# Performance work log

Hardware: AMD Instinct MI355X
Metric: run time of the kernel (lower is better)

Reference implementation:

```python
import jax, jax.numpy as jnp
import numpy as np
from jax import lax

SAMPLE_RATE = 44100.0

def _shelf_coeffs(gain_db, fc, q, sr, high):
    # RBJ cookbook shelf biquad; high=True -> high_shelf, else low_shelf
    A = 10.0 ** (gain_db / 40.0)
    w0 = 2.0 * jnp.pi * (fc / sr)
    alpha = jnp.sin(w0) / (2.0 * q)
    c = jnp.cos(w0)
    sA = jnp.sqrt(A)
    sgn = 1.0 if high else -1.0
    b0 = A * (A + 1 + sgn * (A - 1) * c + 2 * sA * alpha)
    b1 = -2.0 * sgn * A * (A - 1 + sgn * (A + 1) * c)
    b2 = A * (A + 1 + sgn * (A - 1) * c - 2 * sA * alpha)
    a0 = A + 1 - sgn * (A - 1) * c + 2 * sA * alpha
    a1 = 2.0 * sgn * (A - 1 - sgn * (A + 1) * c)
    a2 = A + 1 - sgn * (A - 1) * c - 2 * sA * alpha
    b = jnp.stack([b0, b1, b2]) / a0
    a = jnp.stack([a0, a1, a2]) / a0
    return b, a

def _peaking_coeffs(gain_db, fc, q, sr):
    A = 10.0 ** (gain_db / 40.0)
    w0 = 2.0 * jnp.pi * (fc / sr)
    alpha = jnp.sin(w0) / (2.0 * q)
    c = jnp.cos(w0)
    b0 = 1 + alpha * A
    b1 = -2.0 * c
    b2 = 1 - alpha * A
    a0 = 1 + alpha / A
    a1 = -2.0 * c
    a2 = 1 - alpha / A
    b = jnp.stack([b0, b1, b2]) / a0
    a = jnp.stack([a0, a1, a2]) / a0
    return b, a

def _biquad_lfilter(b, a, x):
    # scipy.signal.lfilter with zero initial conditions, transposed DF-II.
    # x: (chs, T); state s: (chs, 2)
    b0, b1, b2 = b[0], b[1], b[2]
    a1, a2 = a[1], a[2]
    def step(s, xn):  # xn: (chs,)
        s1, s2 = s[:, 0], s[:, 1]
        yn = b0 * xn + s1
        s1n = b1 * xn - a1 * yn + s2
        s2n = b2 * xn - a2 * yn
        return jnp.stack([s1n, s2n], axis=1), yn
    s0 = jnp.zeros((x.shape[0], 2), x.dtype)
    _, y = lax.scan(step, s0, x.T)  # y: (T, chs)
    return y.T

def setup_inputs() -> dict:
    key = jax.random.key(0)
    x = jax.random.normal(key, (8, 2097152), dtype=jnp.float32)
    # rows: [low_shelf, band1, band2, band3, high_shelf]; cols: [gain_db, cutoff_hz, Q]
    eq_params = jnp.array([
        [3.0, 100.0, 0.9],
        [-2.5, 400.0, 1.2],
        [4.0, 1000.0, 2.0],
        [-5.0, 4000.0, 0.7],
        [2.5, 12000.0, 0.707],
    ], dtype=jnp.float32)
    return {"x": x, "eq_params": eq_params}

def reference(x, eq_params):
    sr = SAMPLE_RATE
    # low shelf
    b, a = _shelf_coeffs(eq_params[0, 0], eq_params[0, 1], eq_params[0, 2], sr, high=False)
    y = _biquad_lfilter(b, a, x)
    # 3 peaking bands
    for i in range(1, 4):
        b, a = _peaking_coeffs(eq_params[i, 0], eq_params[i, 1], eq_params[i, 2], sr)
        y = _biquad_lfilter(b, a, y)
    # high shelf
    b, a = _shelf_coeffs(eq_params[4, 0], eq_params[4, 1], eq_params[4, 2], sr, high=True)
    y = _biquad_lfilter(b, a, y)
    return y.astype(jnp.float32)
```

## Files before the change

kernel.cpp:

```cpp
#include <hip/hip_runtime.h>

#define SRATE 44100.0
#ifndef M_PI
#define M_PI 3.14159265358979323846
#endif

#define THREADS 256
#define NBLK 2048
#define STRIDE 17

__device__ __forceinline__ void matvec_tri(const float* __restrict__ M,
                                           const float* bs, float* acc) {
    #pragma unroll
    for (int i = 0; i < 5; i++) {
        #pragma unroll
        for (int h = 0; h < 2; h++) {
            const int r = 2*i + h;
            float a = acc[r];
            #pragma unroll
            for (int k = 0; k < 2*i + 2; k++)
                a = fmaf(M[r*10 + k], bs[k], a);
            acc[r] = a;
        }
    }
}

__device__ __forceinline__ float cascade5(const float* cb0, const float* cb1,
                                          const float* cb2, const float* ca1,
                                          const float* ca2, float* s, float u) {
    #pragma unroll
    for (int st = 0; st < 5; st++) {
        float y  = fmaf(cb0[st], u, s[2*st]);
        float t1 = fmaf(cb1[st], u, s[2*st+1]);
        s[2*st+1] = fmaf(-ca2[st], y, cb2[st] * u);
        s[2*st]   = fmaf(-ca1[st], y, t1);
        u = y;
    }
    return u;
}

__global__ __launch_bounds__(128) void k0_setup(const float* __restrict__ eqp,
                                                float* __restrict__ coef_f,
                                                float* __restrict__ mats_f) {
    __shared__ double cfd[25];
    __shared__ double Md[100];
    int t = threadIdx.x;

    if (t < 5) {
        int i = t;
        double g  = (double)eqp[i*3 + 0];
        double fc = (double)eqp[i*3 + 1];
        double q  = (double)eqp[i*3 + 2];
        double A  = pow(10.0, g / 40.0);
        double w0 = 2.0 * M_PI * (fc / SRATE);
        double al = sin(w0) / (2.0 * q);
        double c  = cos(w0);
        double b0, b1, b2, a0, a1, a2;
        if (i == 0 || i == 4) {
            double sgn = (i == 4) ? 1.0 : -1.0;
            double sA = sqrt(A);
            b0 = A * ((A + 1.0) + sgn * (A - 1.0) * c + 2.0 * sA * al);
            b1 = -2.0 * sgn * A * ((A - 1.0) + sgn * (A + 1.0) * c);
            b2 = A * ((A + 1.0) + sgn * (A - 1.0) * c - 2.0 * sA * al);
            a0 = (A + 1.0) - sgn * (A - 1.0) * c + 2.0 * sA * al;
            a1 = 2.0 * sgn * ((A - 1.0) - sgn * (A + 1.0) * c);
            a2 = (A + 1.0) - sgn * (A - 1.0) * c - 2.0 * sA * al;
        } else {
            b0 = 1.0 + al * A; b1 = -2.0 * c; b2 = 1.0 - al * A;
            a0 = 1.0 + al / A; a1 = -2.0 * c; a2 = 1.0 - al / A;
        }
        cfd[i*5+0] = b0/a0; cfd[i*5+1] = b1/a0; cfd[i*5+2] = b2/a0;
        cfd[i*5+3] = a1/a0; cfd[i*5+4] = a2/a0;
        coef_f[i*5+0] = (float)(b0/a0); coef_f[i*5+1] = (float)(b1/a0);
        coef_f[i*5+2] = (float)(b2/a0); coef_f[i*5+3] = (float)(a1/a0);
        coef_f[i*5+4] = (float)(a2/a0);
    }
    __syncthreads();

    if (t < 10) {
        double s[10];
        #pragma unroll
        for (int k = 0; k < 10; k++) s[k] = (k == t) ? 1.0 : 0.0;
        double u = 0.0;
        #pragma unroll
        for (int i = 0; i < 5; i++) {
            double y   = cfd[i*5+0] * u + s[2*i];
            double s1n = cfd[i*5+1] * u - cfd[i*5+3] * y + s[2*i+1];
            double s2n = cfd[i*5+2] * u - cfd[i*5+4] * y;
            s[2*i] = s1n; s[2*i+1] = s2n; u = y;
        }
        for (int r = 0; r < 10; r++) Md[r*10 + t] = s[r];
    }
    __syncthreads();

    for (int k = 1; k <= 20; k++) {
        double val = 0.0;
        if (t < 100) {
            int r = t / 10, c = t % 10;
            #pragma unroll
            for (int j = 0; j < 10; j++) val += Md[r*10 + j] * Md[j*10 + c];
        }
        __syncthreads();
        if (t < 100) {
            Md[t] = val;
            int d = k - 5;
            if (d >= 0 && d < 16) mats_f[d*100 + t] = (float)val;
        }
        __syncthreads();
    }
}

__global__ __launch_bounds__(256, 6) void kA(const float* __restrict__ x,
                                             const float* __restrict__ coef,
                                             const float* __restrict__ mats,
                                             float* __restrict__ ibuf,
                                             float* __restrict__ abuf) {
    __shared__ union {
        float stage[256 * STRIDE];
        float buf[256][11];
    } sm;
    __shared__ float Mf[800];
    __shared__ float cfs[25];
    const int t = threadIdx.x, b = blockIdx.x;
    const int cb = t >> 2, q = t & 3;
    const float4* x4 = (const float4*)x + (size_t)b * 2048;

    float4 rr[4];
    #pragma unroll
    for (int k = 0; k < 4; k++) rr[k] = x4[(cb + 64*k)*8 + q];

    for (int i = t; i < 800; i += 256) Mf[i] = mats[i];
    if (t < 25) cfs[t] = coef[t];

    #pragma unroll
    for (int k = 0; k < 4; k++) {
        int o = (cb + 64*k)*STRIDE + q*4;
        sm.stage[o+0]=rr[k].x; sm.stage[o+1]=rr[k].y;
        sm.stage[o+2]=rr[k].z; sm.stage[o+3]=rr[k].w;
    }
    __syncthreads();

    #pragma unroll
    for (int k = 0; k < 4; k++) rr[k] = x4[(cb + 64*k)*8 + 4 + q];

    float cb0[5],cb1[5],cb2[5],ca1[5],ca2[5];
    #pragma unroll
    for (int i = 0; i < 5; i++) {
        cb0[i]=cfs[i*5+0]; cb1[i]=cfs[i*5+1]; cb2[i]=cfs[i*5+2];
        ca1[i]=cfs[i*5+3]; ca2[i]=cfs[i*5+4];
    }

    float s[10];
    #pragma unroll
    for (int k = 0; k < 10; k++) s[k] = 0.0f;

    {
        const float* row = sm.stage + t*STRIDE;
        #pragma unroll
        for (int i = 0; i < 16; i++) (void)cascade5(cb0,cb1,cb2,ca1,ca2, s, row[i]);
    }
    __syncthreads();
    #pragma unroll
    for (int k = 0; k < 4; k++) {
        int o = (cb + 64*k)*STRIDE + q*4;
        sm.stage[o+0]=rr[k].x; sm.stage[o+1]=rr[k].y;
        sm.stage[o+2]=rr[k].z; sm.stage[o+3]=rr[k].w;
    }
    __syncthreads();
    {
        const float* row = sm.stage + t*STRIDE;
        #pragma unroll
        for (int i = 0; i < 16; i++) (void)cascade5(cb0,cb1,cb2,ca1,ca2, s, row[i]);
    }
    __syncthreads();

    #pragma unroll
    for (int r = 0; r < 10; r++) sm.buf[t][r] = s[r];
    __syncthreads();

    #pragma unroll 1
    for (int d = 0; d < 8; d++) {
        int src = t - (1 << d);
        int sc  = src < 0 ? 0 : src;
        float bs[10], nv[10];
        #pragma unroll
        for (int r = 0; r < 10; r++) { bs[r] = sm.buf[sc][r]; nv[r] = s[r]; }
        matvec_tri(&Mf[d*100], bs, nv);
        __syncthreads();
        bool act = src >= 0;
        #pragma unroll
        for (int r = 0; r < 10; r++) { s[r] = act ? nv[r] : s[r]; sm.buf[t][r] = s[r]; }
        __syncthreads();
    }

    #pragma unroll
    for (int r = 0; r < 10; r++)
        ibuf[(size_t)b * 2560 + r * 256 + t] = (t > 0) ? sm.buf[t-1][r] : 0.0f;
    if (t == 255) {
        #pragma unroll
        for (int r = 0; r < 10; r++) abuf[b * 10 + r] = s[r];
    }
}

__global__ __launch_bounds__(256) void kB(const float* __restrict__ mats,
                                          const float* __restrict__ abuf,
                                          float* __restrict__ bbuf) {
    __shared__ float Qf[800];
    __shared__ float buf[256][11];
    const int t = threadIdx.x, ch = blockIdx.x;
    const int g = ch * 256 + t;

    for (int i = t; i < 800; i += 256) Qf[i] = mats[800 + i];

    float v[10];
    #pragma unroll
    for (int r = 0; r < 10; r++) { v[r] = abuf[g * 10 + r]; buf[t][r] = v[r]; }
    __syncthreads();

    #pragma unroll 1
    for (int e = 0; e < 8; e++) {
        int src = t - (1 << e);
        int sc  = src < 0 ? 0 : src;
        float bs[10], nv[10];
        #pragma unroll
        for (int r = 0; r < 10; r++) { bs[r] = buf[sc][r]; nv[r] = v[r]; }
        matvec_tri(&Qf[e*100], bs, nv);
        __syncthreads();
        bool act = src >= 0;
        #pragma unroll
        for (int r = 0; r < 10; r++) { v[r] = act ? nv[r] : v[r]; buf[t][r] = v[r]; }
        __syncthreads();
    }

    #pragma unroll
    for (int r = 0; r < 10; r++)
        bbuf[g * 10 + r] = (t > 0) ? buf[t-1][r] : 0.0f;
}

__global__ __launch_bounds__(256, 6) void kC(const float* __restrict__ x,
                                             const float* __restrict__ coef,
                                             const float* __restrict__ mats,
                                             const float* __restrict__ ibuf,
                                             const float* __restrict__ bbuf,
                                             float* __restrict__ out) {
    __shared__ float stage[256 * STRIDE];
    __shared__ float Mf[800];
    __shared__ float cfs[25];
    const int t = threadIdx.x, b = blockIdx.x;
    const int cb = t >> 2, q = t & 3;
    const float4* x4 = (const float4*)x + (size_t)b * 2048;
    float4* o4 = (float4*)out + (size_t)b * 2048;

    float4 rr[4];
    #pragma unroll
    for (int k = 0; k < 4; k++) rr[k] = x4[(cb + 64*k)*8 + q];

    float sp[10];
    #pragma unroll
    for (int r = 0; r < 10; r++) sp[r] = ibuf[(size_t)b * 2560 + r * 256 + t];
    float bp[10];
    #pragma unroll
    for (int r = 0; r < 10; r++) bp[r] = bbuf[b * 10 + r];

    for (int i = t; i < 800; i += 256) Mf[i] = mats[i];
    if (t < 25) cfs[t] = coef[t];

    #pragma unroll
    for (int k = 0; k < 4; k++) {
        int o = (cb + 64*k)*STRIDE + q*4;
        stage[o+0]=rr[k].x; stage[o+1]=rr[k].y;
        stage[o+2]=rr[k].z; stage[o+3]=rr[k].w;
    }
    __syncthreads();

    #pragma unroll
    for (int k = 0; k < 4; k++) rr[k] = x4[(cb + 64*k)*8 + 4 + q];

    float cb0[5],cb1[5],cb2[5],ca1[5],ca2[5];
    #pragma unroll
    for (int i = 0; i < 5; i++) {
        cb0[i]=cfs[i*5+0]; cb1[i]=cfs[i*5+1]; cb2[i]=cfs[i*5+2];
        ca1[i]=cfs[i*5+3]; ca2[i]=cfs[i*5+4];
    }

    #pragma unroll 1
    for (int d = 0; d < 8; d++) {
        float wv[10];
        #pragma unroll
        for (int r = 0; r < 10; r++) wv[r] = 0.0f;
        matvec_tri(&Mf[d*100], bp, wv);
        bool bit = (t >> d) & 1;
        #pragma unroll
        for (int r = 0; r < 10; r++) bp[r] = bit ? wv[r] : bp[r];
    }
    float s[10];
    #pragma unroll
    for (int r = 0; r < 10; r++) s[r] = sp[r] + bp[r];

    {
        float* row = stage + t*STRIDE;
        #pragma unroll
        for (int i = 0; i < 16; i++) row[i] = cascade5(cb0,cb1,cb2,ca1,ca2, s, row[i]);
    }
    __syncthreads();
    #pragma unroll
    for (int k = 0; k < 4; k++) {
        int o = (cb + 64*k)*STRIDE + q*4;
        o4[(cb + 64*k)*8 + q] = make_float4(stage[o+0], stage[o+1], stage[o+2], stage[o+3]);
    }
    __syncthreads();
    #pragma unroll
    for (int k = 0; k < 4; k++) {
        int o = (cb + 64*k)*STRIDE + q*4;
        stage[o+0]=rr[k].x; stage[o+1]=rr[k].y;
        stage[o+2]=rr[k].z; stage[o+3]=rr[k].w;
    }
    __syncthreads();
    {
        float* row = stage + t*STRIDE;
        #pragma unroll
        for (int i = 0; i < 16; i++) row[i] = cascade5(cb0,cb1,cb2,ca1,ca2, s, row[i]);
    }
    __syncthreads();
    #pragma unroll
    for (int k = 0; k < 4; k++) {
        int o = (cb + 64*k)*STRIDE + q*4;
        o4[(cb + 64*k)*8 + 4 + q] = make_float4(stage[o+0], stage[o+1], stage[o+2], stage[o+3]);
    }
}

extern "C" void kernel_launch(void* const* d_in, const int* in_sizes, int n_in,
                              void* d_out, int out_size, void* d_ws, size_t ws_size,
                              hipStream_t stream) {
    const float* x   = (const float*)d_in[0];
    const float* eqp = (const float*)d_in[1];
    float* out = (float*)d_out;
    char* ws = (char*)d_ws;

    float* coef_f = (float*)ws;
    float* mats_f = (float*)(ws + 256);
    float* ibuf   = (float*)(ws + 8192);
    float* abuf   = (float*)(ws + 8192 + 20971520);
    float* bbuf   = (float*)(ws + 8192 + 20971520 + 81920);

    hipLaunchKernelGGL(k0_setup, dim3(1), dim3(128), 0, stream, eqp, coef_f, mats_f);
    hipLaunchKernelGGL(kA, dim3(NBLK), dim3(THREADS), 0, stream, x, coef_f, mats_f, ibuf, abuf);
    hipLaunchKernelGGL(kB, dim3(8),    dim3(THREADS), 0, stream, mats_f, abuf, bbuf);
    hipLaunchKernelGGL(kC, dim3(NBLK), dim3(THREADS), 0, stream,
                       x, coef_f, mats_f, ibuf, bbuf, out);
}
```

Baseline: 190.1 us.

## Recompute intra-block prefix states in kC instead of round-tripping ibuf

kA no longer writes the per-thread exclusive prefix states (about 20 MB) to global memory. Its block-level scan becomes a reduction-only up-sweep that produces just the block aggregate. kC now reruns the local cascade and the full Hillis-Steele scan itself, keeping input in registers to avoid a second global read, and writes output through a double shared-memory stage with fewer barriers. This removes a large global write and read in exchange for duplicated compute in kC, more registers, more shared memory, and a lower launch-bounds occupancy hint.

```diff
diff --git a/kernel.cpp b/kernel.cpp
--- a/kernel.cpp
+++ b/kernel.cpp
@@ -110,24 +110,26 @@
     }
 }
 
-__global__ __launch_bounds__(256, 6) void kA(const float* __restrict__ x,
+__global__ __launch_bounds__(256, 4) void kA(const float* __restrict__ x,
                                              const float* __restrict__ coef,
                                              const float* __restrict__ mats,
-                                             float* __restrict__ ibuf,
                                              float* __restrict__ abuf) {
     __shared__ union {
-        float stage[256 * STRIDE];
+        float s0[256 * STRIDE];
         float buf[256][11];
-    } sm;
+    } smA;
+    __shared__ float s1[256 * STRIDE];
     __shared__ float Mf[800];
     __shared__ float cfs[25];
     const int t = threadIdx.x, b = blockIdx.x;
     const int cb = t >> 2, q = t & 3;
     const float4* x4 = (const float4*)x + (size_t)b * 2048;
 
-    float4 rr[4];
-    #pragma unroll
-    for (int k = 0; k < 4; k++) rr[k] = x4[(cb + 64*k)*8 + q];
+    float4 rr[4], rr2[4];
+    #pragma unroll
+    for (int k = 0; k < 4; k++) rr[k]  = x4[(cb + 64*k)*8 + q];
+    #pragma unroll
+    for (int k = 0; k < 4; k++) rr2[k] = x4[(cb + 64*k)*8 + 4 + q];
 
     for (int i = t; i < 800; i += 256) Mf[i] = mats[i];
     if (t < 25) cfs[t] = coef[t];
@@ -135,13 +137,17 @@
     #pragma unroll
     for (int k = 0; k < 4; k++) {
         int o = (cb + 64*k)*STRIDE + q*4;
-        sm.stage[o+0]=rr[k].x; sm.stage[o+1]=rr[k].y;
-        sm.stage[o+2]=rr[k].z; sm.stage[o+3]=rr[k].w;
-    }
-    __syncthreads();
-
-    #pragma unroll
-    for (int k = 0; k < 4; k++) rr[k] = x4[(cb + 64*k)*8 + 4 + q];
+        smA.s0[o+0]=rr[k].x; smA.s0[o+1]=rr[k].y;
+        smA.s0[o+2]=rr[k].z; smA.s0[o+3]=rr[k].w;
+    }
+    __syncthreads();
+
+    #pragma unroll
+    for (int k = 0; k < 4; k++) {
+        int o = (cb + 64*k)*STRIDE + q*4;
+        s1[o+0]=rr2[k].x; s1[o+1]=rr2[k].y;
+        s1[o+2]=rr2[k].z; s1[o+3]=rr2[k].w;
+    }
 
     float cb0[5],cb1[5],cb2[5],ca1[5],ca2[5];
     #pragma unroll
@@ -154,48 +160,35 @@
     #pragma unroll
     for (int k = 0; k < 10; k++) s[k] = 0.0f;
 
-    {
-        const float* row = sm.stage + t*STRIDE;
+    {   const float* row = smA.s0 + t*STRIDE;
         #pragma unroll
         for (int i = 0; i < 16; i++) (void)cascade5(cb0,cb1,cb2,ca1,ca2, s, row[i]);
     }
     __syncthreads();
-    #pragma unroll
-    for (int k = 0; k < 4; k++) {
-        int o = (cb + 64*k)*STRIDE + q*4;
-        sm.stage[o+0]=rr[k].x; sm.stage[o+1]=rr[k].y;
-        sm.stage[o+2]=rr[k].z; sm.stage[o+3]=rr[k].w;
-    }
-    __syncthreads();
-    {
-        const float* row = sm.stage + t*STRIDE;
+    {   const float* row = s1 + t*STRIDE;
         #pragma unroll
         for (int i = 0; i < 16; i++) (void)cascade5(cb0,cb1,cb2,ca1,ca2, s, row[i]);
     }
-    __syncthreads();
-
-    #pragma unroll
-    for (int r = 0; r < 10; r++) sm.buf[t][r] = s[r];
+
+    #pragma unroll
+    for (int r = 0; r < 10; r++) smA.buf[t][r] = s[r];
     __syncthreads();
 
     #pragma unroll 1
     for (int d = 0; d < 8; d++) {
-        int src = t - (1 << d);
-        int sc  = src < 0 ? 0 : src;
-        float bs[10], nv[10];
-        #pragma unroll
-        for (int r = 0; r < 10; r++) { bs[r] = sm.buf[sc][r]; nv[r] = s[r]; }
-        matvec_tri(&Mf[d*100], bs, nv);
-        __syncthreads();
-        bool act = src >= 0;
-        #pragma unroll
-        for (int r = 0; r < 10; r++) { s[r] = act ? nv[r] : s[r]; sm.buf[t][r] = s[r]; }
-        __syncthreads();
-    }
-
-    #pragma unroll
-    for (int r = 0; r < 10; r++)
-        ibuf[(size_t)b * 2560 + r * 256 + t] = (t > 0) ? sm.buf[t-1][r] : 0.0f;
+        const int span = 2 << d;
+        if (((t + 1) & (span - 1)) == 0) {
+            const int partner = t - (1 << d);
+            float bs[10];
+            #pragma unroll
+            for (int r = 0; r < 10; r++) bs[r] = smA.buf[partner][r];
+            matvec_tri(&Mf[d*100], bs, s);
+            #pragma unroll
+            for (int r = 0; r < 10; r++) smA.buf[t][r] = s[r];
+        }
+        __syncthreads();
+    }
+
     if (t == 255) {
         #pragma unroll
         for (int r = 0; r < 10; r++) abuf[b * 10 + r] = s[r];
@@ -237,13 +230,16 @@
         bbuf[g * 10 + r] = (t > 0) ? buf[t-1][r] : 0.0f;
 }
 
-__global__ __launch_bounds__(256, 6) void kC(const float* __restrict__ x,
+__global__ __launch_bounds__(256, 4) void kC(const float* __restrict__ x,
                                              const float* __restrict__ coef,
                                              const float* __restrict__ mats,
-                                             const float* __restrict__ ibuf,
                                              const float* __restrict__ bbuf,
                                              float* __restrict__ out) {
-    __shared__ float stage[256 * STRIDE];
+    __shared__ union {
+        float s0[256 * STRIDE];
+        float buf[256][11];
+    } smA;
+    __shared__ float s1[256 * STRIDE];
     __shared__ float Mf[800];
     __shared__ float cfs[25];
     const int t = threadIdx.x, b = blockIdx.x;
@@ -251,30 +247,33 @@
     const float4* x4 = (const float4*)x + (size_t)b * 2048;
     float4* o4 = (float4*)out + (size_t)b * 2048;
 
-    float4 rr[4];
-    #pragma unroll
-    for (int k = 0; k < 4; k++) rr[k] = x4[(cb + 64*k)*8 + q];
-
-    float sp[10];
-    #pragma unroll
-    for (int r = 0; r < 10; r++) sp[r] = ibuf[(size_t)b * 2560 + r * 256 + t];
-    float bp[10];
-    #pragma unroll
-    for (int r = 0; r < 10; r++) bp[r] = bbuf[b * 10 + r];
+    float4 rr[4], rr2[4];
+    #pragma unroll
+    for (int k = 0; k < 4; k++) rr[k]  = x4[(cb + 64*k)*8 + q];
+    #pragma unroll
+    for (int k = 0; k < 4; k++) rr2[k] = x4[(cb + 64*k)*8 + 4 + q];
 
     for (int i = t; i < 800; i += 256) Mf[i] = mats[i];
     if (t < 25) cfs[t] = coef[t];
 
+    float bp[10];
+    #pragma unroll
+    for (int r = 0; r < 10; r++) bp[r] = bbuf[b * 10 + r];
+
     #pragma unroll
     for (int k = 0; k < 4; k++) {
         int o = (cb + 64*k)*STRIDE + q*4;
-        stage[o+0]=rr[k].x; stage[o+1]=rr[k].y;
-        stage[o+2]=rr[k].z; stage[o+3]=rr[k].w;
-    }
-    __syncthreads();
-
-    #pragma unroll
-    for (int k = 0; k < 4; k++) rr[k] = x4[(cb + 64*k)*8 + 4 + q];
+        smA.s0[o+0]=rr[k].x; smA.s0[o+1]=rr[k].y;
+        smA.s0[o+2]=rr[k].z; smA.s0[o+3]=rr[k].w;
+    }
+    __syncthreads();
+
+    #pragma unroll
+    for (int k = 0; k < 4; k++) {
+        int o = (cb + 64*k)*STRIDE + q*4;
+        s1[o+0]=rr2[k].x; s1[o+1]=rr2[k].y;
+        s1[o+2]=rr2[k].z; s1[o+3]=rr2[k].w;
+    }
 
     float cb0[5],cb1[5],cb2[5],ca1[5],ca2[5];
     #pragma unroll
@@ -283,6 +282,43 @@
         ca1[i]=cfs[i*5+3]; ca2[i]=cfs[i*5+4];
     }
 
+    float xw0[16], xw1[16];
+    float s[10];
+    #pragma unroll
+    for (int k = 0; k < 10; k++) s[k] = 0.0f;
+    {   const float* row = smA.s0 + t*STRIDE;
+        #pragma unroll
+        for (int i = 0; i < 16; i++) { xw0[i] = row[i]; (void)cascade5(cb0,cb1,cb2,ca1,ca2, s, xw0[i]); }
+    }
+    __syncthreads();
+    {   const float* row = s1 + t*STRIDE;
+        #pragma unroll
+        for (int i = 0; i < 16; i++) { xw1[i] = row[i]; (void)cascade5(cb0,cb1,cb2,ca1,ca2, s, xw1[i]); }
+    }
+
+    #pragma unroll
+    for (int r = 0; r < 10; r++) smA.buf[t][r] = s[r];
+    __syncthreads();
+
+    #pragma unroll 1
+    for (int d = 0; d < 8; d++) {
+        int src = t - (1 << d);
+        int sc  = src < 0 ? 0 : src;
+        float bs[10], nv[10];
+        #pragma unroll
+        for (int r = 0; r < 10; r++) { bs[r] = smA.buf[sc][r]; nv[r] = s[r]; }
+        matvec_tri(&Mf[d*100], bs, nv);
+        __syncthreads();
+        bool act = src >= 0;
+        #pragma unroll
+        for (int r = 0; r < 10; r++) { s[r] = act ? nv[r] : s[r]; smA.buf[t][r] = s[r]; }
+        __syncthreads();
+    }
+
+    float sp[10];
+    #pragma unroll
+    for (int r = 0; r < 10; r++) sp[r] = (t > 0) ? smA.buf[t-1][r] : 0.0f;
+
     #pragma unroll 1
     for (int d = 0; d < 8; d++) {
         float wv[10];
@@ -293,39 +329,32 @@
         #pragma unroll
         for (int r = 0; r < 10; r++) bp[r] = bit ? wv[r] : bp[r];
     }
-    float s[10];
     #pragma unroll
     for (int r = 0; r < 10; r++) s[r] = sp[r] + bp[r];
-
-    {
-        float* row = stage + t*STRIDE;
-        #pragma unroll
-        for (int i = 0; i < 16; i++) row[i] = cascade5(cb0,cb1,cb2,ca1,ca2, s, row[i]);
-    }
-    __syncthreads();
-    #pragma unroll
-    for (int k = 0; k < 4; k++) {
-        int o = (cb + 64*k)*STRIDE + q*4;
-        o4[(cb + 64*k)*8 + q] = make_float4(stage[o+0], stage[o+1], stage[o+2], stage[o+3]);
-    }
-    __syncthreads();
-    #pragma unroll
-    for (int k = 0; k < 4; k++) {
-        int o = (cb + 64*k)*STRIDE + q*4;
-        stage[o+0]=rr[k].x; stage[o+1]=rr[k].y;
-        stage[o+2]=rr[k].z; stage[o+3]=rr[k].w;
-    }
-    __syncthreads();
-    {
-        float* row = stage + t*STRIDE;
-        #pragma unroll
-        for (int i = 0; i < 16; i++) row[i] = cascade5(cb0,cb1,cb2,ca1,ca2, s, row[i]);
-    }
-    __syncthreads();
-    #pragma unroll
-    for (int k = 0; k < 4; k++) {
-        int o = (cb + 64*k)*STRIDE + q*4;
-        o4[(cb + 64*k)*8 + 4 + q] = make_float4(stage[o+0], stage[o+1], stage[o+2], stage[o+3]);
+    __syncthreads();
+
+    #pragma unroll
+    for (int i = 0; i < 16; i++) xw0[i] = cascade5(cb0,cb1,cb2,ca1,ca2, s, xw0[i]);
+    #pragma unroll
+    for (int i = 0; i < 16; i++) xw1[i] = cascade5(cb0,cb1,cb2,ca1,ca2, s, xw1[i]);
+
+    {   float* row = smA.s0 + t*STRIDE;
+        #pragma unroll
+        for (int i = 0; i < 16; i++) row[i] = xw0[i];
+    }
+    {   float* row = s1 + t*STRIDE;
+        #pragma unroll
+        for (int i = 0; i < 16; i++) row[i] = xw1[i];
+    }
+    __syncthreads();
+
+    const int c2 = t >> 3, p = t & 7, pq = p & 3;
+    const float* srcb = (p < 4) ? smA.s0 : s1;
+    #pragma unroll
+    for (int kk = 0; kk < 8; kk++) {
+        int chunk = c2 + 32*kk;
+        int o = chunk*STRIDE + pq*4;
+        o4[chunk*8 + p] = make_float4(srcb[o+0], srcb[o+1], srcb[o+2], srcb[o+3]);
     }
 }
 
@@ -339,13 +368,12 @@
 
     float* coef_f = (float*)ws;
     float* mats_f = (float*)(ws + 256);
-    float* ibuf   = (float*)(ws + 8192);
-    float* abuf   = (float*)(ws + 8192 + 20971520);
-    float* bbuf   = (float*)(ws + 8192 + 20971520 + 81920);
+    float* abuf   = (float*)(ws + 8192);
+    float* bbuf   = (float*)(ws + 8192 + 81920);
 
     hipLaunchKernelGGL(k0_setup, dim3(1), dim3(128), 0, stream, eqp, coef_f, mats_f);
-    hipLaunchKernelGGL(kA, dim3(NBLK), dim3(THREADS), 0, stream, x, coef_f, mats_f, ibuf, abuf);
+    hipLaunchKernelGGL(kA, dim3(NBLK), dim3(THREADS), 0, stream, x, coef_f, mats_f, abuf);
     hipLaunchKernelGGL(kB, dim3(8),    dim3(THREADS), 0, stream, mats_f, abuf, bbuf);
     hipLaunchKernelGGL(kC, dim3(NBLK), dim3(THREADS), 0, stream,
-                       x, coef_f, mats_f, ibuf, bbuf, out);
-}
+                       x, coef_f, mats_f, bbuf, out);
+}
```

After: 191.6 us. Within noise of the previous version (+0.8%).
